# Optimization experiments

Measured on AMD Instinct MI355X. Metric: run time of the kernel, lower is better.

## Reference

```python
import jax, jax.numpy as jnp
import numpy as np

N_NODES = 20000
N_EDGES = 100000
D_IN = 768
NEG_SLOPE = 0.2  # DGL GATConv default


def _gat_layer(x, W, attn_l, attn_r, bias, src, dst, num_heads, head_dim, use_elu):
    N = x.shape[0]
    z = (x @ W).reshape(N, num_heads, head_dim)          # [N,H,D]
    el = jnp.sum(z * attn_l, axis=-1)                    # [N,H]
    er = jnp.sum(z * attn_r, axis=-1)                    # [N,H]
    e = jax.nn.leaky_relu(el[src] + er[dst], NEG_SLOPE)  # [E,H]
    # segment softmax over incoming edges of each dst node
    m = jax.ops.segment_max(e, dst, num_segments=N)      # [N,H] (-inf for isolated nodes, never gathered)
    ex = jnp.exp(e - m[dst])                             # [E,H]
    denom = jax.ops.segment_sum(ex, dst, num_segments=N) # [N,H]
    alpha = ex / denom[dst]                              # [E,H]
    msg = alpha[:, :, None] * z[src]                     # [E,H,D]
    out = jax.ops.segment_sum(msg, dst, num_segments=N)  # [N,H,D]
    out = out + z                                        # identity residual (in == H*D)
    out = out + bias.reshape(1, num_heads, head_dim)
    if use_elu:
        out = jax.nn.elu(out)
    return out.reshape(N, num_heads * head_dim)


def setup_inputs() -> dict:
    key = jax.random.key(0)
    ks = jax.random.split(key, 16)
    node_features = jax.random.normal(ks[0], (N_NODES, D_IN), dtype=jnp.float32)
    src = jax.random.randint(ks[1], (N_EDGES,), 0, N_NODES)
    dst = jax.random.randint(ks[2], (N_EDGES,), 0, N_NODES)
    s = 1.0 / np.sqrt(D_IN)
    inp = {"node_features": node_features, "src": src, "dst": dst}
    # layers 0,1: H=12, D=64; layer 2: H=1, D=768
    heads = [(12, 64), (12, 64), (1, 768)]
    for i, (H, D) in enumerate(heads):
        inp[f"W{i}"] = jax.random.normal(ks[3 + 4 * i], (D_IN, H * D), dtype=jnp.float32) * s
        inp[f"al{i}"] = jax.random.normal(ks[4 + 4 * i], (H, D), dtype=jnp.float32) * s
        inp[f"ar{i}"] = jax.random.normal(ks[5 + 4 * i], (H, D), dtype=jnp.float32) * s
        inp[f"b{i}"] = jnp.zeros((H * D,), dtype=jnp.float32)
    return inp


def reference(node_features, W0, al0, ar0, b0, W1, al1, ar1, b1, W2, al2, ar2, b2, src, dst):
    x = _gat_layer(node_features, W0, al0, ar0, b0, src, dst, 12, 64, True)
    x = _gat_layer(x, W1, al1, ar1, b1, src, dst, 12, 64, True)
    x = _gat_layer(x, W2, al2, ar2, b2, src, dst, 1, 768, False)
    return x
```

## Files before the change

### kernel.cpp

```cpp
#include <hip/hip_runtime.h>
#include <cstdint>
#include <cstddef>

#define DINL __device__ __forceinline__

typedef __attribute__((ext_vector_type(8))) short bf16x8;
typedef __attribute__((ext_vector_type(4))) float f32x4;

DINL unsigned f32_ord(float f) {
    unsigned u = __float_as_uint(f);
    return (u & 0x80000000u) ? ~u : (u | 0x80000000u);
}
DINL float ord_f32(unsigned v) {
    return (v & 0x80000000u) ? __uint_as_float(v & 0x7FFFFFFFu)
                             : __uint_as_float(~v);
}

DINL unsigned short f2bf(float f) {
    unsigned u = __float_as_uint(f);
    unsigned r = u + 0x7FFFu + ((u >> 16) & 1u);
    return (unsigned short)(r >> 16);
}
DINL float bf2f(unsigned short h) { return __uint_as_float((unsigned)h << 16); }

#define GLOAD_LDS16(g, l)                                                     \
    __builtin_amdgcn_global_load_lds(                                         \
        (const __attribute__((address_space(1))) void*)(g),                   \
        (__attribute__((address_space(3))) void*)(l), 16, 0, 0)

__global__ void decompose_a(const float* __restrict__ x,
                            unsigned short* __restrict__ hi,
                            unsigned short* __restrict__ lo,
                            int Nrows, int Mpad) {
    int i4 = blockIdx.x * blockDim.x + threadIdx.x;
    int total = Mpad * 192;
    if (i4 >= total) return;
    int row = i4 / 192;
    float4 v = (row < Nrows) ? ((const float4*)x)[i4]
                             : make_float4(0.f, 0.f, 0.f, 0.f);
    ushort4 h, l;
    h.x = f2bf(v.x); l.x = f2bf(v.x - bf2f(h.x));
    h.y = f2bf(v.y); l.y = f2bf(v.y - bf2f(h.y));
    h.z = f2bf(v.z); l.z = f2bf(v.z - bf2f(h.z));
    h.w = f2bf(v.w); l.w = f2bf(v.w - bf2f(h.w));
    ((ushort4*)hi)[i4] = h;
    ((ushort4*)lo)[i4] = l;
}

__global__ __launch_bounds__(256) void decompose_bT(const float* __restrict__ W,
                                                    unsigned short* __restrict__ hiT,
                                                    unsigned short* __restrict__ loT) {
    __shared__ float tile[64][65];
    int k0 = blockIdx.x * 64, n0 = blockIdx.y * 64;
    int t = threadIdx.x;
#pragma unroll
    for (int i = 0; i < 16; ++i) {
        int idx = t + i * 256;
        int r = idx >> 6, c = idx & 63;
        tile[r][c] = W[(size_t)(k0 + r) * 768 + n0 + c];
    }
    __syncthreads();
#pragma unroll
    for (int i = 0; i < 16; ++i) {
        int idx = t + i * 256;
        int r = idx >> 6, c = idx & 63;
        float v = tile[c][r];
        unsigned short h = f2bf(v);
        hiT[(size_t)(n0 + r) * 768 + k0 + c] = h;
        loT[(size_t)(n0 + r) * 768 + k0 + c] = f2bf(v - bf2f(h));
    }
}

__global__ __launch_bounds__(256) void gemm_fused_bf16(
        const unsigned short* __restrict__ Ahi, const unsigned short* __restrict__ Alo,
        const unsigned short* __restrict__ BThi, const unsigned short* __restrict__ BTlo,
        float* __restrict__ C,
        const float* __restrict__ attl, const float* __restrict__ attr,
        float* __restrict__ el, float* __restrict__ er,
        int Nrows, int do_attn) {
    constexpr int K = 768, NC = 768, BKK = 32, NT = K / BKK;
    __shared__ __align__(16) unsigned short AsH[2][128 * BKK];
    __shared__ __align__(16) unsigned short AsL[2][128 * BKK];
    __shared__ __align__(16) unsigned short BsH[2][128 * BKK];
    __shared__ __align__(16) unsigned short BsL[2][128 * BKK];
    const int t = threadIdx.x, w = t >> 6, l = t & 63;
    const int m0 = blockIdx.x * 128, n0 = blockIdx.y * 128;
    const int wr = w >> 1, wc = w & 1;

    f32x4 acc[4][4] = {};

    const int srow = w * 16 + (l >> 2);
    const int scol = (l & 3) * 8;
    const int kr = (l >> 4) * 8;

    auto stage = [&](int buf, int k0) {
#pragma unroll
        for (int c = 0; c < 2; ++c) {
            const size_t ga = (size_t)(m0 + c * 64 + srow) * K + k0 + scol;
            const size_t gb = (size_t)(n0 + c * 64 + srow) * K + k0 + scol;
            const int lofs = (c * 64 + w * 16) * BKK;
            GLOAD_LDS16(Ahi + ga, &AsH[buf][lofs]);
            GLOAD_LDS16(Alo + ga, &AsL[buf][lofs]);
            GLOAD_LDS16(BThi + gb, &BsH[buf][lofs]);
            GLOAD_LDS16(BTlo + gb, &BsL[buf][lofs]);
        }
    };

    stage(0, 0);
    asm volatile("s_waitcnt vmcnt(0)" ::: "memory");
    __builtin_amdgcn_s_barrier();

    for (int tt = 0; tt < NT; ++tt) {
        const int cur = tt & 1;
        if (tt < NT - 1) stage(cur ^ 1, (tt + 1) * BKK);

        bf16x8 fbh[4], fbl[4];
#pragma unroll
        for (int j = 0; j < 4; ++j) {
            const int row = (wc * 64 + j * 16 + (l & 15)) * BKK + kr;
            fbh[j] = *(const bf16x8*)&BsH[cur][row];
            fbl[j] = *(const bf16x8*)&BsL[cur][row];
        }
        __builtin_amdgcn_s_setprio(1);
#pragma unroll
        for (int i = 0; i < 4; ++i) {
            const int row = (wr * 64 + i * 16 + (l & 15)) * BKK + kr;
            bf16x8 fah = *(const bf16x8*)&AsH[cur][row];
            bf16x8 fal = *(const bf16x8*)&AsL[cur][row];
#pragma unroll
            for (int j = 0; j < 4; ++j) {
                acc[i][j] = __builtin_amdgcn_mfma_f32_16x16x32_bf16(fah, fbh[j], acc[i][j], 0, 0, 0);
                acc[i][j] = __builtin_amdgcn_mfma_f32_16x16x32_bf16(fah, fbl[j], acc[i][j], 0, 0, 0);
                acc[i][j] = __builtin_amdgcn_mfma_f32_16x16x32_bf16(fal, fbh[j], acc[i][j], 0, 0, 0);
            }
        }
        __builtin_amdgcn_s_setprio(0);

        asm volatile("s_waitcnt vmcnt(0)" ::: "memory");
        __builtin_amdgcn_s_barrier();
    }

    const int crow = m0 + wr * 64 + (l >> 4) * 4;
    const int ccol = n0 + wc * 64 + (l & 15);
#pragma unroll
    for (int i = 0; i < 4; ++i)
#pragma unroll
        for (int j = 0; j < 4; ++j)
#pragma unroll
            for (int r = 0; r < 4; ++r)
                C[(size_t)(crow + i * 16 + r) * NC + ccol + j * 16] = acc[i][j][r];

    if (do_attn) {
        const int h = blockIdx.y * 2 + wc;
        float alc[4], arc[4];
#pragma unroll
        for (int j = 0; j < 4; ++j) {
            alc[j] = attl[h * 64 + (l & 15) + j * 16];
            arc[j] = attr[h * 64 + (l & 15) + j * 16];
        }
#pragma unroll
        for (int i = 0; i < 4; ++i)
#pragma unroll
            for (int r = 0; r < 4; ++r) {
                float sl = 0.f, sr = 0.f;
#pragma unroll
                for (int j = 0; j < 4; ++j) {
                    sl += acc[i][j][r] * alc[j];
                    sr += acc[i][j][r] * arc[j];
                }
#pragma unroll
                for (int o = 1; o < 16; o <<= 1) {
                    sl += __shfl_xor(sl, o);
                    sr += __shfl_xor(sr, o);
                }
                int row = crow + i * 16 + r;
                if ((l & 15) == 0 && row < Nrows) {
                    el[row * 12 + h] = sl;
                    er[row * 12 + h] = sr;
                }
            }
    }
}

__global__ __launch_bounds__(256) void el_er_kernel(const float* __restrict__ z,
                                                    const float* __restrict__ al,
                                                    const float* __restrict__ ar,
                                                    float* __restrict__ el,
                                                    float* __restrict__ er,
                                                    int N, int H, int Dh) {
    int wid = (blockIdx.x * 256 + threadIdx.x) >> 6;
    int lane = threadIdx.x & 63;
    if (wid >= N * H) return;
    int n = wid / H, h = wid % H;
    const float* zr = z + (size_t)n * (H * Dh) + h * Dh;
    const float* alr = al + h * Dh;
    const float* arr = ar + h * Dh;
    float sl = 0.f, sr = 0.f;
    for (int d = lane; d < Dh; d += 64) {
        float zv = zr[d];
        sl += zv * alr[d];
        sr += zv * arr[d];
    }
#pragma unroll
    for (int o = 32; o; o >>= 1) {
        sl += __shfl_down(sl, o);
        sr += __shfl_down(sr, o);
    }
    if (lane == 0) { el[wid] = sl; er[wid] = sr; }
}

__global__ void init_mdenom(unsigned* __restrict__ m, float* __restrict__ denom, int n) {
    int i = blockIdx.x * blockDim.x + threadIdx.x;
    if (i < n) { m[i] = 0u; denom[i] = 0.f; }
}

__global__ void edge_e_kernel(const int* __restrict__ src, const int* __restrict__ dst,
                              const float* __restrict__ el, const float* __restrict__ er,
                              float* __restrict__ e, unsigned* __restrict__ m,
                              int E, int H) {
    int i = blockIdx.x * blockDim.x + threadIdx.x;
    if (i >= E * H) return;
    int ed = i / H, h = i - ed * H;
    int s = src[ed], d = dst[ed];
    float v = el[s * H + h] + er[d * H + h];
    v = (v >= 0.f) ? v : 0.2f * v;
    e[i] = v;
    atomicMax(&m[d * H + h], f32_ord(v));
}

__global__ void edge_ex_kernel(const int* __restrict__ dst,
                               float* __restrict__ e, const unsigned* __restrict__ m,
                               float* __restrict__ denom, int E, int H) {
    int i = blockIdx.x * blockDim.x + threadIdx.x;
    if (i >= E * H) return;
    int ed = i / H, h = i - ed * H;
    int d = dst[ed];
    float x = expf(e[i] - ord_f32(m[d * H + h]));
    e[i] = x;
    atomicAdd(&denom[d * H + h], x);
}

__global__ void csr_zero(int* __restrict__ counts, int* __restrict__ cursor, int N) {
    int i = blockIdx.x * blockDim.x + threadIdx.x;
    if (i < N) { counts[i] = 0; cursor[i] = 0; }
}

__global__ void csr_count(const int* __restrict__ dst, int* __restrict__ counts, int E) {
    int i = blockIdx.x * blockDim.x + threadIdx.x;
    if (i < E) atomicAdd(&counts[dst[i]], 1);
}

__global__ __launch_bounds__(1024) void csr_scan(const int* __restrict__ counts,
                                                 int* __restrict__ offsets, int N, int E) {
    __shared__ int part[1024];
    const int t = threadIdx.x;
    const int CH = (N + 1023) / 1024;
    const int base = t * CH;
    int s = 0;
    for (int i = 0; i < CH; ++i) {
        int idx = base + i;
        if (idx < N) s += counts[idx];
    }
    part[t] = s;
    __syncthreads();
    for (int o = 1; o < 1024; o <<= 1) {
        int v = (t >= o) ? part[t - o] : 0;
        __syncthreads();
        part[t] += v;
        __syncthreads();
    }
    int run = (t > 0) ? part[t - 1] : 0;
    for (int i = 0; i < CH; ++i) {
        int idx = base + i;
        if (idx < N) { offsets[idx] = run; run += counts[idx]; }
    }
    if (t == 1023) offsets[N] = E;
}

__global__ void csr_scatter(const int* __restrict__ src, const int* __restrict__ dst,
                            const int* __restrict__ offsets, int* __restrict__ cursor,
                            int* __restrict__ perm, int* __restrict__ psrc, int E) {
    int e = blockIdx.x * blockDim.x + threadIdx.x;
    if (e >= E) return;
    int d = dst[e];
    int pos = offsets[d] + atomicAdd(&cursor[d], 1);
    perm[pos] = e;
    psrc[pos] = src[e];
}

__global__ __launch_bounds__(256) void aggregate_csr(const int* __restrict__ offsets,
                                                     const int* __restrict__ perm,
                                                     const int* __restrict__ psrc,
                                                     const float* __restrict__ z,
                                                     const float* __restrict__ ex,
                                                     const float* __restrict__ denom,
                                                     const float* __restrict__ bias,
                                                     float* __restrict__ out,
                                                     unsigned short* __restrict__ nAhi,
                                                     unsigned short* __restrict__ nAlo,
                                                     int N, int Mpad, int H, int Dh,
                                                     int use_elu, int mode) {
    int d = (blockIdx.x * 256 + threadIdx.x) >> 6;
    int lane = threadIdx.x & 63;
    int limit = mode ? Mpad : N;
    if (d >= limit) return;

    if (d >= N) {
        ushort4 zz = {0, 0, 0, 0};
#pragma unroll
        for (int q = 0; q < 3; ++q) {
            ((ushort4*)nAhi)[(size_t)d * 192 + lane + 64 * q] = zz;
            ((ushort4*)nAlo)[(size_t)d * 192 + lane + 64 * q] = zz;
        }
        return;
    }

    float inv_den = 0.f;
    if (lane < H) inv_den = 1.0f / denom[d * H + lane];

    const float4* zd = (const float4*)(z + (size_t)d * 768);
    const float4* bv = (const float4*)bias;
    float4 acc[3];
#pragma unroll
    for (int q = 0; q < 3; ++q) {
        float4 a = zd[lane + 64 * q];
        float4 b = bv[lane + 64 * q];
        acc[q] = make_float4(a.x + b.x, a.y + b.y, a.z + b.z, a.w + b.w);
    }

    const int beg = offsets[d], end = offsets[d + 1];
    for (int p = beg; p < end; ++p) {
        int e = perm[p];
        int s = psrc[p];
        float alpha = 0.f;
        if (lane < H) alpha = ex[(size_t)e * H + lane] * inv_den;
        const float4* zs = (const float4*)(z + (size_t)s * 768);
#pragma unroll
        for (int q = 0; q < 3; ++q) {
            int idx = lane + 64 * q;
            int h = (4 * idx) / Dh;
            float a = __shfl(alpha, h);
            float4 zv = zs[idx];
            acc[q].x += a * zv.x;
            acc[q].y += a * zv.y;
            acc[q].z += a * zv.z;
            acc[q].w += a * zv.w;
        }
    }

#pragma unroll
    for (int q = 0; q < 3; ++q) {
        float4 v = acc[q];
        if (use_elu) {
            v.x = v.x > 0.f ? v.x : expm1f(v.x);
            v.y = v.y > 0.f ? v.y : expm1f(v.y);
            v.z = v.z > 0.f ? v.z : expm1f(v.z);
            v.w = v.w > 0.f ? v.w : expm1f(v.w);
        }
        if (mode) {
            ushort4 h4, l4;
            h4.x = f2bf(v.x); l4.x = f2bf(v.x - bf2f(h4.x));
            h4.y = f2bf(v.y); l4.y = f2bf(v.y - bf2f(h4.y));
            h4.z = f2bf(v.z); l4.z = f2bf(v.z - bf2f(h4.z));
            h4.w = f2bf(v.w); l4.w = f2bf(v.w - bf2f(h4.w));
            ((ushort4*)nAhi)[(size_t)d * 192 + lane + 64 * q] = h4;
            ((ushort4*)nAlo)[(size_t)d * 192 + lane + 64 * q] = l4;
        } else {
            ((float4*)(out + (size_t)d * 768))[lane + 64 * q] = v;
        }
    }
}

static void run_layer(const float* W, const float* al, const float* ar,
                      const float* bias, const int* src, const int* dst,
                      const int* offsets, const int* perm, const int* psrc,
                      unsigned short* Ahi, unsigned short* Alo,
                      unsigned short* BThi, unsigned short* BTlo,
                      float* z, float* out, float* ebuf, float* el, float* er,
                      unsigned* m, float* denom,
                      int N, int Mpad, int E, int H, int Dh, bool use_elu, int mode,
                      hipStream_t stream) {
    decompose_bT<<<dim3(12, 12), 256, 0, stream>>>(W, BThi, BTlo);
    gemm_fused_bf16<<<dim3(Mpad / 128, 6), 256, 0, stream>>>(
        Ahi, Alo, BThi, BTlo, z, al, ar, el, er, N, H == 12 ? 1 : 0);
    if (H != 12)
        el_er_kernel<<<(N * H * 64 + 255) / 256, 256, 0, stream>>>(z, al, ar, el, er, N, H, Dh);
    init_mdenom<<<(N * H + 255) / 256, 256, 0, stream>>>(m, denom, N * H);
    edge_e_kernel<<<(E * H + 255) / 256, 256, 0, stream>>>(src, dst, el, er, ebuf, m, E, H);
    edge_ex_kernel<<<(E * H + 255) / 256, 256, 0, stream>>>(dst, ebuf, m, denom, E, H);
    int waves = mode ? Mpad : N;
    aggregate_csr<<<(waves * 64 + 255) / 256, 256, 0, stream>>>(
        offsets, perm, psrc, z, ebuf, denom, bias, out, Ahi, Alo,
        N, Mpad, H, Dh, use_elu ? 1 : 0, mode);
}

extern "C" void kernel_launch(void* const* d_in, const int* in_sizes, int n_in,
                              void* d_out, int out_size, void* d_ws, size_t ws_size,
                              hipStream_t stream) {
    const float* x0 = (const float*)d_in[0];
    const int* src = (const int*)d_in[1];
    const int* dst = (const int*)d_in[2];
    const float* W[3]  = {(const float*)d_in[3], (const float*)d_in[7],  (const float*)d_in[11]};
    const float* al[3] = {(const float*)d_in[4], (const float*)d_in[8],  (const float*)d_in[12]};
    const float* ar[3] = {(const float*)d_in[5], (const float*)d_in[9],  (const float*)d_in[13]};
    const float* bs[3] = {(const float*)d_in[6], (const float*)d_in[10], (const float*)d_in[14]};

    const int N = in_sizes[0] / 768;
    const int E = in_sizes[1];
    const int Mpad = ((N + 127) / 128) * 128;

    char* p = (char*)d_ws;
    const size_t FP = (size_t)Mpad * 768 * sizeof(float);
    const size_t BF = (size_t)Mpad * 768 * sizeof(unsigned short);
    float* z = (float*)p;                 p += FP;
    unsigned short* Ahi = (unsigned short*)p;  p += BF;
    unsigned short* Alo = (unsigned short*)p;  p += BF;
    unsigned short* BThi = (unsigned short*)p; p += (size_t)768 * 768 * 2;
    unsigned short* BTlo = (unsigned short*)p; p += (size_t)768 * 768 * 2;
    float* ebuf = (float*)p;              p += (size_t)E * 12 * sizeof(float);
    float* el = (float*)p;                p += (size_t)N * 12 * sizeof(float);
    float* er = (float*)p;                p += (size_t)N * 12 * sizeof(float);
    unsigned* m = (unsigned*)p;           p += (size_t)N * 12 * sizeof(unsigned);
    float* denom = (float*)p;             p += (size_t)N * 12 * sizeof(float);
    int* counts = (int*)p;                p += (size_t)N * sizeof(int);
    int* cursor = (int*)p;                p += (size_t)N * sizeof(int);
    int* offsets = (int*)p;               p += (size_t)(N + 4) * sizeof(int);
    int* perm = (int*)p;                  p += (size_t)E * sizeof(int);
    int* psrc = (int*)p;                  p += (size_t)E * sizeof(int);

    csr_zero<<<(N + 255) / 256, 256, 0, stream>>>(counts, cursor, N);
    csr_count<<<(E + 255) / 256, 256, 0, stream>>>(dst, counts, E);
    csr_scan<<<1, 1024, 0, stream>>>(counts, offsets, N, E);
    csr_scatter<<<(E + 255) / 256, 256, 0, stream>>>(src, dst, offsets, cursor, perm, psrc, E);

    decompose_a<<<(Mpad * 192 + 255) / 256, 256, 0, stream>>>(x0, Ahi, Alo, N, Mpad);

    run_layer(W[0], al[0], ar[0], bs[0], src, dst, offsets, perm, psrc,
              Ahi, Alo, BThi, BTlo, z, nullptr, ebuf, el, er, m, denom,
              N, Mpad, E, 12, 64, true, 1, stream);
    run_layer(W[1], al[1], ar[1], bs[1], src, dst, offsets, perm, psrc,
              Ahi, Alo, BThi, BTlo, z, nullptr, ebuf, el, er, m, denom,
              N, Mpad, E, 12, 64, true, 1, stream);
    run_layer(W[2], al[2], ar[2], bs[2], src, dst, offsets, perm, psrc,
              Ahi, Alo, BThi, BTlo, z, (float*)d_out, ebuf, el, er, m, denom,
              N, Mpad, E, 1, 768, false, 0, stream);
}
```

Baseline: 743.6 us.

## Use 512-thread GEMM blocks, CSR-ordered edge buffers, and split aggregation across three waves

The GEMM block grows to 512 threads (8 waves), with each wave covering 32 rows instead of 64 and each staging a single chunk. Accumulator registers per wave drop, which should raise occupancy. Edge score and exp kernels now iterate in CSR (dst-sorted) order, so the aggregation reads attention values contiguously and the perm indirection goes away. Aggregation uses three waves per node, each handling a 256-float slice with a 2-edge unrolled loop, which adds parallelism but makes each wave re-read the per-edge indices and alphas.

After: 708.5 us. 1.05x faster.

```diff
diff --git a/kernel.cpp b/kernel.cpp
--- a/kernel.cpp
+++ b/kernel.cpp
@@ -71,7 +71,7 @@
     }
 }
 
-__global__ __launch_bounds__(256) void gemm_fused_bf16(
+__global__ __launch_bounds__(512) void gemm_fused_bf16(
         const unsigned short* __restrict__ Ahi, const unsigned short* __restrict__ Alo,
         const unsigned short* __restrict__ BThi, const unsigned short* __restrict__ BTlo,
         float* __restrict__ C,
@@ -87,23 +87,20 @@
     const int m0 = blockIdx.x * 128, n0 = blockIdx.y * 128;
     const int wr = w >> 1, wc = w & 1;
 
-    f32x4 acc[4][4] = {};
+    f32x4 acc[2][4] = {};
 
     const int srow = w * 16 + (l >> 2);
     const int scol = (l & 3) * 8;
     const int kr = (l >> 4) * 8;
 
     auto stage = [&](int buf, int k0) {
-#pragma unroll
-        for (int c = 0; c < 2; ++c) {
-            const size_t ga = (size_t)(m0 + c * 64 + srow) * K + k0 + scol;
-            const size_t gb = (size_t)(n0 + c * 64 + srow) * K + k0 + scol;
-            const int lofs = (c * 64 + w * 16) * BKK;
-            GLOAD_LDS16(Ahi + ga, &AsH[buf][lofs]);
-            GLOAD_LDS16(Alo + ga, &AsL[buf][lofs]);
-            GLOAD_LDS16(BThi + gb, &BsH[buf][lofs]);
-            GLOAD_LDS16(BTlo + gb, &BsL[buf][lofs]);
-        }
+        const size_t ga = (size_t)(m0 + srow) * K + k0 + scol;
+        const size_t gb = (size_t)(n0 + srow) * K + k0 + scol;
+        const int lofs = (w * 16) * BKK;
+        GLOAD_LDS16(Ahi + ga, &AsH[buf][lofs]);
+        GLOAD_LDS16(Alo + ga, &AsL[buf][lofs]);
+        GLOAD_LDS16(BThi + gb, &BsH[buf][lofs]);
+        GLOAD_LDS16(BTlo + gb, &BsL[buf][lofs]);
     };
 
     stage(0, 0);
@@ -123,8 +120,8 @@
         }
         __builtin_amdgcn_s_setprio(1);
 #pragma unroll
-        for (int i = 0; i < 4; ++i) {
-            const int row = (wr * 64 + i * 16 + (l & 15)) * BKK + kr;
+        for (int i = 0; i < 2; ++i) {
+            const int row = (wr * 32 + i * 16 + (l & 15)) * BKK + kr;
             bf16x8 fah = *(const bf16x8*)&AsH[cur][row];
             bf16x8 fal = *(const bf16x8*)&AsL[cur][row];
 #pragma unroll
@@ -140,10 +137,10 @@
         __builtin_amdgcn_s_barrier();
     }
 
-    const int crow = m0 + wr * 64 + (l >> 4) * 4;
+    const int crow = m0 + wr * 32 + (l >> 4) * 4;
     const int ccol = n0 + wc * 64 + (l & 15);
 #pragma unroll
-    for (int i = 0; i < 4; ++i)
+    for (int i = 0; i < 2; ++i)
 #pragma unroll
         for (int j = 0; j < 4; ++j)
 #pragma unroll
@@ -159,7 +156,7 @@
             arc[j] = attr[h * 64 + (l & 15) + j * 16];
         }
 #pragma unroll
-        for (int i = 0; i < 4; ++i)
+        for (int i = 0; i < 2; ++i)
 #pragma unroll
             for (int r = 0; r < 4; ++r) {
                 float sl = 0.f, sr = 0.f;
@@ -214,27 +211,27 @@
     if (i < n) { m[i] = 0u; denom[i] = 0.f; }
 }
 
-__global__ void edge_e_kernel(const int* __restrict__ src, const int* __restrict__ dst,
+__global__ void edge_e_kernel(const int* __restrict__ psrc, const int* __restrict__ pdst,
                               const float* __restrict__ el, const float* __restrict__ er,
                               float* __restrict__ e, unsigned* __restrict__ m,
                               int E, int H) {
     int i = blockIdx.x * blockDim.x + threadIdx.x;
     if (i >= E * H) return;
-    int ed = i / H, h = i - ed * H;
-    int s = src[ed], d = dst[ed];
+    int p = i / H, h = i - p * H;
+    int s = psrc[p], d = pdst[p];
     float v = el[s * H + h] + er[d * H + h];
     v = (v >= 0.f) ? v : 0.2f * v;
     e[i] = v;
     atomicMax(&m[d * H + h], f32_ord(v));
 }
 
-__global__ void edge_ex_kernel(const int* __restrict__ dst,
+__global__ void edge_ex_kernel(const int* __restrict__ pdst,
                                float* __restrict__ e, const unsigned* __restrict__ m,
                                float* __restrict__ denom, int E, int H) {
     int i = blockIdx.x * blockDim.x + threadIdx.x;
     if (i >= E * H) return;
-    int ed = i / H, h = i - ed * H;
-    int d = dst[ed];
+    int p = i / H, h = i - p * H;
+    int d = pdst[p];
     float x = expf(e[i] - ord_f32(m[d * H + h]));
     e[i] = x;
     atomicAdd(&denom[d * H + h], x);
@@ -279,17 +276,16 @@
 
 __global__ void csr_scatter(const int* __restrict__ src, const int* __restrict__ dst,
                             const int* __restrict__ offsets, int* __restrict__ cursor,
-                            int* __restrict__ perm, int* __restrict__ psrc, int E) {
+                            int* __restrict__ psrc, int* __restrict__ pdst, int E) {
     int e = blockIdx.x * blockDim.x + threadIdx.x;
     if (e >= E) return;
     int d = dst[e];
     int pos = offsets[d] + atomicAdd(&cursor[d], 1);
-    perm[pos] = e;
     psrc[pos] = src[e];
+    pdst[pos] = d;
 }
 
 __global__ __launch_bounds__(256) void aggregate_csr(const int* __restrict__ offsets,
-                                                     const int* __restrict__ perm,
                                                      const int* __restrict__ psrc,
                                                      const float* __restrict__ z,
                                                      const float* __restrict__ ex,
@@ -300,80 +296,80 @@
                                                      unsigned short* __restrict__ nAlo,
                                                      int N, int Mpad, int H, int Dh,
                                                      int use_elu, int mode) {
-    int d = (blockIdx.x * 256 + threadIdx.x) >> 6;
+    int wid = (blockIdx.x * 256 + threadIdx.x) >> 6;
     int lane = threadIdx.x & 63;
     int limit = mode ? Mpad : N;
+    int d = wid / 3, q = wid - d * 3;
     if (d >= limit) return;
+    const int idx = lane + 64 * q;
 
     if (d >= N) {
         ushort4 zz = {0, 0, 0, 0};
-#pragma unroll
-        for (int q = 0; q < 3; ++q) {
-            ((ushort4*)nAhi)[(size_t)d * 192 + lane + 64 * q] = zz;
-            ((ushort4*)nAlo)[(size_t)d * 192 + lane + 64 * q] = zz;
-        }
+        ((ushort4*)nAhi)[(size_t)d * 192 + idx] = zz;
+        ((ushort4*)nAlo)[(size_t)d * 192 + idx] = zz;
         return;
     }
 
     float inv_den = 0.f;
     if (lane < H) inv_den = 1.0f / denom[d * H + lane];
-
-    const float4* zd = (const float4*)(z + (size_t)d * 768);
-    const float4* bv = (const float4*)bias;
-    float4 acc[3];
-#pragma unroll
-    for (int q = 0; q < 3; ++q) {
-        float4 a = zd[lane + 64 * q];
-        float4 b = bv[lane + 64 * q];
-        acc[q] = make_float4(a.x + b.x, a.y + b.y, a.z + b.z, a.w + b.w);
-    }
+    const int h = (4 * idx) / Dh;
+
+    float4 a = ((const float4*)(z + (size_t)d * 768))[idx];
+    float4 b = ((const float4*)bias)[idx];
+    float4 acc = make_float4(a.x + b.x, a.y + b.y, a.z + b.z, a.w + b.w);
 
     const int beg = offsets[d], end = offsets[d + 1];
-    for (int p = beg; p < end; ++p) {
-        int e = perm[p];
-        int s = psrc[p];
-        float alpha = 0.f;
-        if (lane < H) alpha = ex[(size_t)e * H + lane] * inv_den;
-        const float4* zs = (const float4*)(z + (size_t)s * 768);
-#pragma unroll
-        for (int q = 0; q < 3; ++q) {
-            int idx = lane + 64 * q;
-            int h = (4 * idx) / Dh;
-            float a = __shfl(alpha, h);
-            float4 zv = zs[idx];
-            acc[q].x += a * zv.x;
-            acc[q].y += a * zv.y;
-            acc[q].z += a * zv.z;
-            acc[q].w += a * zv.w;
+    int p = beg;
+    for (; p + 1 < end; p += 2) {
+        int s0 = psrc[p], s1 = psrc[p + 1];
+        float al0 = 0.f, al1 = 0.f;
+        if (lane < H) {
+            al0 = ex[(size_t)p * H + lane] * inv_den;
+            al1 = ex[(size_t)(p + 1) * H + lane] * inv_den;
         }
-    }
-
-#pragma unroll
-    for (int q = 0; q < 3; ++q) {
-        float4 v = acc[q];
-        if (use_elu) {
-            v.x = v.x > 0.f ? v.x : expm1f(v.x);
-            v.y = v.y > 0.f ? v.y : expm1f(v.y);
-            v.z = v.z > 0.f ? v.z : expm1f(v.z);
-            v.w = v.w > 0.f ? v.w : expm1f(v.w);
-        }
-        if (mode) {
-            ushort4 h4, l4;
-            h4.x = f2bf(v.x); l4.x = f2bf(v.x - bf2f(h4.x));
-            h4.y = f2bf(v.y); l4.y = f2bf(v.y - bf2f(h4.y));
-            h4.z = f2bf(v.z); l4.z = f2bf(v.z - bf2f(h4.z));
-            h4.w = f2bf(v.w); l4.w = f2bf(v.w - bf2f(h4.w));
-            ((ushort4*)nAhi)[(size_t)d * 192 + lane + 64 * q] = h4;
-            ((ushort4*)nAlo)[(size_t)d * 192 + lane + 64 * q] = l4;
-        } else {
-            ((float4*)(out + (size_t)d * 768))[lane + 64 * q] = v;
-        }
+        float4 z0 = ((const float4*)(z + (size_t)s0 * 768))[idx];
+        float4 z1 = ((const float4*)(z + (size_t)s1 * 768))[idx];
+        float aa0 = __shfl(al0, h), aa1 = __shfl(al1, h);
+        acc.x += aa0 * z0.x + aa1 * z1.x;
+        acc.y += aa0 * z0.y + aa1 * z1.y;
+        acc.z += aa0 * z0.z + aa1 * z1.z;
+        acc.w += aa0 * z0.w + aa1 * z1.w;
+    }
+    if (p < end) {
+        int s0 = psrc[p];
+        float al0 = 0.f;
+        if (lane < H) al0 = ex[(size_t)p * H + lane] * inv_den;
+        float4 z0 = ((const float4*)(z + (size_t)s0 * 768))[idx];
+        float aa0 = __shfl(al0, h);
+        acc.x += aa0 * z0.x;
+        acc.y += aa0 * z0.y;
+        acc.z += aa0 * z0.z;
+        acc.w += aa0 * z0.w;
+    }
+
+    float4 v = acc;
+    if (use_elu) {
+        v.x = v.x > 0.f ? v.x : expm1f(v.x);
+        v.y = v.y > 0.f ? v.y : expm1f(v.y);
+        v.z = v.z > 0.f ? v.z : expm1f(v.z);
+        v.w = v.w > 0.f ? v.w : expm1f(v.w);
+    }
+    if (mode) {
+        ushort4 h4, l4;
+        h4.x = f2bf(v.x); l4.x = f2bf(v.x - bf2f(h4.x));
+        h4.y = f2bf(v.y); l4.y = f2bf(v.y - bf2f(h4.y));
+        h4.z = f2bf(v.z); l4.z = f2bf(v.z - bf2f(h4.z));
+        h4.w = f2bf(v.w); l4.w = f2bf(v.w - bf2f(h4.w));
+        ((ushort4*)nAhi)[(size_t)d * 192 + idx] = h4;
+        ((ushort4*)nAlo)[(size_t)d * 192 + idx] = l4;
+    } else {
+        ((float4*)(out + (size_t)d * 768))[idx] = v;
     }
 }
 
 static void run_layer(const float* W, const float* al, const float* ar,
-                      const float* bias, const int* src, const int* dst,
-                      const int* offsets, const int* perm, const int* psrc,
+                      const float* bias,
+                      const int* offsets, const int* psrc, const int* pdst,
                       unsigned short* Ahi, unsigned short* Alo,
                       unsigned short* BThi, unsigned short* BTlo,
                       float* z, float* out, float* ebuf, float* el, float* er,
@@ -381,16 +377,16 @@
                       int N, int Mpad, int E, int H, int Dh, bool use_elu, int mode,
                       hipStream_t stream) {
     decompose_bT<<<dim3(12, 12), 256, 0, stream>>>(W, BThi, BTlo);
-    gemm_fused_bf16<<<dim3(Mpad / 128, 6), 256, 0, stream>>>(
+    gemm_fused_bf16<<<dim3(Mpad / 128, 6), 512, 0, stream>>>(
         Ahi, Alo, BThi, BTlo, z, al, ar, el, er, N, H == 12 ? 1 : 0);
     if (H != 12)
         el_er_kernel<<<(N * H * 64 + 255) / 256, 256, 0, stream>>>(z, al, ar, el, er, N, H, Dh);
     init_mdenom<<<(N * H + 255) / 256, 256, 0, stream>>>(m, denom, N * H);
-    edge_e_kernel<<<(E * H + 255) / 256, 256, 0, stream>>>(src, dst, el, er, ebuf, m, E, H);
-    edge_ex_kernel<<<(E * H + 255) / 256, 256, 0, stream>>>(dst, ebuf, m, denom, E, H);
-    int waves = mode ? Mpad : N;
-    aggregate_csr<<<(waves * 64 + 255) / 256, 256, 0, stream>>>(
-        offsets, perm, psrc, z, ebuf, denom, bias, out, Ahi, Alo,
+    edge_e_kernel<<<(E * H + 255) / 256, 256, 0, stream>>>(psrc, pdst, el, er, ebuf, m, E, H);
+    edge_ex_kernel<<<(E * H + 255) / 256, 256, 0, stream>>>(pdst, ebuf, m, denom, E, H);
+    int limit = mode ? Mpad : N;
+    aggregate_csr<<<((size_t)limit * 3 * 64 + 255) / 256, 256, 0, stream>>>(
+        offsets, psrc, z, ebuf, denom, bias, out, Ahi, Alo,
         N, Mpad, H, Dh, use_elu ? 1 : 0, mode);
 }
 
@@ -425,23 +421,23 @@
     int* counts = (int*)p;                p += (size_t)N * sizeof(int);
     int* cursor = (int*)p;                p += (size_t)N * sizeof(int);
     int* offsets = (int*)p;               p += (size_t)(N + 4) * sizeof(int);
-    int* perm = (int*)p;                  p += (size_t)E * sizeof(int);
     int* psrc = (int*)p;                  p += (size_t)E * sizeof(int);
+    int* pdst = (int*)p;                  p += (size_t)E * sizeof(int);
 
     csr_zero<<<(N + 255) / 256, 256, 0, stream>>>(counts, cursor, N);
     csr_count<<<(E + 255) / 256, 256, 0, stream>>>(dst, counts, E);
     csr_scan<<<1, 1024, 0, stream>>>(counts, offsets, N, E);
-    csr_scatter<<<(E + 255) / 256, 256, 0, stream>>>(src, dst, offsets, cursor, perm, psrc, E);
+    csr_scatter<<<(E + 255) / 256, 256, 0, stream>>>(src, dst, offsets, cursor, psrc, pdst, E);
 
     decompose_a<<<(Mpad * 192 + 255) / 256, 256, 0, stream>>>(x0, Ahi, Alo, N, Mpad);
 
-    run_layer(W[0], al[0], ar[0], bs[0], src, dst, offsets, perm, psrc,
+    run_layer(W[0], al[0], ar[0], bs[0], offsets, psrc, pdst,
               Ahi, Alo, BThi, BTlo, z, nullptr, ebuf, el, er, m, denom,
               N, Mpad, E, 12, 64, true, 1, stream);
-    run_layer(W[1], al[1], ar[1], bs[1], src, dst, offsets, perm, psrc,
+    run_layer(W[1], al[1], ar[1], bs[1], offsets, psrc, pdst,
               Ahi, Alo, BThi, BTlo, z, nullptr, ebuf, el, er, m, denom,
               N, Mpad, E, 12, 64, true, 1, stream);
-    run_layer(W[2], al[2], ar[2], bs[2], src, dst, offsets, perm, psrc,
+    run_layer(W[2], al[2], ar[2], bs[2], offsets, psrc, pdst,
               Ahi, Alo, BThi, BTlo, z, (float*)d_out, ebuf, el, er, m, denom,
               N, Mpad, E, 1, 768, false, 0, stream);
 }
```
